# Optimization experiments

Measured on AMD Instinct MI355X. Metric: run time of the kernel, lower is better.

Reference implementation:

```python
import jax, jax.numpy as jnp
import numpy as np

T, H, I = 4096, 4096, 11008  # tokens, hidden_size, intermediate_size
QMAX = 127.0


def setup_inputs() -> dict:
    key = jax.random.key(0)
    k0, k1, k2, k3, k4 = jax.random.split(key, 5)
    x = jax.random.normal(k0, (T, H), dtype=jnp.float32)
    # int8 weights stored as float32 integer values in [-127, 127]
    wq_gate_up = jnp.round(jnp.clip(jax.random.normal(k1, (2 * I, H), dtype=jnp.float32) * 30.0, -QMAX, QMAX))
    s_gate_up = jax.random.uniform(k2, (2 * I,), dtype=jnp.float32, minval=5e-4, maxval=2e-3)
    wq_down = jnp.round(jnp.clip(jax.random.normal(k3, (H, I), dtype=jnp.float32) * 30.0, -QMAX, QMAX))
    s_down = jax.random.uniform(k4, (H,), dtype=jnp.float32, minval=5e-4, maxval=2e-3)
    return {"x": x, "wq_gate_up": wq_gate_up, "s_gate_up": s_gate_up,
            "wq_down": wq_down, "s_down": s_down}


def reference(x, wq_gate_up, s_gate_up, wq_down, s_down):
    # --- quantize activations (per-tensor dynamic int8) ---
    x_scale = jnp.max(jnp.abs(x)) / QMAX
    qx = jnp.clip(jnp.round(x / x_scale), -QMAX, QMAX)  # integer-valued f32 (simulated int8)

    # --- gate_up_proj: int8 GEMM (int32 accumulate simulated in f32) ---
    acc = qx @ wq_gate_up.T                             # [T, 2I]
    gate_up = acc * (x_scale * s_gate_up)               # dequant: per-tensor act * per-channel weight scale

    # --- DequantSiluAndMulQuant: silu(gate) * up, then dynamic requant ---
    gate, up = jnp.split(gate_up, 2, axis=-1)           # [T, I] each
    h = jax.nn.silu(gate) * up
    h_scale = jnp.max(jnp.abs(h)) / QMAX
    qh = jnp.clip(jnp.round(h / h_scale), -QMAX, QMAX)

    # --- down_proj: int8 GEMM + dequant ---
    out = (qh @ wq_down.T) * (h_scale * s_down)         # [T, H]
    return out, h_scale
```

## Files before the change

### kernel.cpp

```cpp
#include <hip/hip_runtime.h>

#define T_DIM 4096
#define K1    4096
#define I_DIM 11008
#define QMAXF 127.0f

typedef int v4i  __attribute__((ext_vector_type(4)));
typedef int v16i __attribute__((ext_vector_type(16)));


__device__ __forceinline__ void gload16(const void* g, void* l) {
  __builtin_amdgcn_global_load_lds((__attribute__((address_space(1))) unsigned int*)(g),
                                   (__attribute__((address_space(3))) unsigned int*)(l),
                                   16, 0, 0);
}

__device__ __forceinline__ int packq(float a, float b, float c, float d) {
  return ((int)a & 255) | (((int)b & 255) << 8) | (((int)c & 255) << 16) | (((int)d & 255) << 24);
}


__global__ void absmax_x_kernel(const float4* __restrict__ x4, unsigned* __restrict__ maxbits, int n4) {
  int tid = blockIdx.x * blockDim.x + threadIdx.x;
  int stride = gridDim.x * blockDim.x;
  float m = 0.f;
  for (int i = tid; i < n4; i += stride) {
    float4 v = x4[i];
    m = fmaxf(m, fmaxf(fmaxf(fabsf(v.x), fabsf(v.y)), fmaxf(fabsf(v.z), fabsf(v.w))));
  }
  #pragma unroll
  for (int off = 32; off; off >>= 1) m = fmaxf(m, __shfl_xor(m, off));
  if ((threadIdx.x & 63) == 0) atomicMax(maxbits, __float_as_uint(m));
}


__global__ void quant_x_kernel(const float4* __restrict__ x4, v4i* __restrict__ q4,
                               const unsigned* __restrict__ scal) {
  const float sx = __uint_as_float(scal[0]) * (1.0f / QMAXF);
  const long i = (long)blockIdx.x * blockDim.x + threadIdx.x;
  v4i o;
  #pragma unroll
  for (int j = 0; j < 4; ++j) {
    float4 v = x4[i * 4 + j];
    float a = fminf(fmaxf(rintf(v.x / sx), -QMAXF), QMAXF);
    float b = fminf(fmaxf(rintf(v.y / sx), -QMAXF), QMAXF);
    float c = fminf(fmaxf(rintf(v.z / sx), -QMAXF), QMAXF);
    float d = fminf(fmaxf(rintf(v.w / sx), -QMAXF), QMAXF);
    o[j] = packq(a, b, c, d);
  }
  q4[i] = o;
}


__global__ void conv_w_kernel(const float4* __restrict__ w4, v4i* __restrict__ q4) {
  const long i = (long)blockIdx.x * blockDim.x + threadIdx.x;
  v4i o;
  #pragma unroll
  for (int j = 0; j < 4; ++j) {
    float4 v = w4[i * 4 + j];
    o[j] = packq(rintf(v.x), rintf(v.y), rintf(v.z), rintf(v.w));
  }
  q4[i] = o;
}


__global__ __launch_bounds__(512, 2)
void gemm1_silu_kernel(const signed char* __restrict__ qx,
                       const signed char* __restrict__ w8,
                       const float* __restrict__ sgu,
                       unsigned* __restrict__ scal,
                       float* __restrict__ hbuf)
{
  __shared__ signed char L[4][32768];

  const int tid  = threadIdx.x;
  const int lane = tid & 63;
  const int wid  = tid >> 6;
  const int wr   = wid >> 1;
  const int wc   = wid & 1;
  const int l31  = lane & 31;
  const int kgl  = lane >> 5;

  const int lin = blockIdx.x;
  const int sw  = (lin & 7) * 172 + (lin >> 3);
  const int brow = (sw & 15) * 256;
  const int bcol = (sw >> 4) * 128;

  const int sr = tid & 255, sk = tid >> 8;
  const signed char* gA = qx + (size_t)(brow + sr) * K1 + sk * 16;
  const int grp = sr >> 6, w = sr & 63;
  const int gcolw = bcol + grp * 32 + (w & 31);
  const size_t srcrow = (w < 32) ? (size_t)gcolw : (size_t)(I_DIM + gcolw);
  const signed char* gB = w8 + srcrow * K1 + sk * 16;
  const int lA = tid * 16;
  const int lB = 16384 + tid * 16;

  const int ab = (wr * 64 + l31) * 16;
  const int bb = 16384 + (wc * 128 + l31) * 16;

  v16i zero = {0};
  v16i acc[2][4];
  #pragma unroll
  for (int m = 0; m < 2; ++m)
    #pragma unroll
    for (int n = 0; n < 4; ++n) acc[m][n] = zero;

  const int nk = K1 / 64;
  #pragma unroll
  for (int t = 0; t < 3; ++t) {
    gload16(gA + t * 64,      &L[t][lA]);
    gload16(gA + t * 64 + 32, &L[t][lA + 8192]);
    gload16(gB + t * 64,      &L[t][lB]);
    gload16(gB + t * 64 + 32, &L[t][lB + 8192]);
  }

  for (int t = 0; t < nk; ++t) {
    if (t + 2 < nk)      asm volatile("s_waitcnt vmcnt(8)" ::: "memory");
    else if (t + 1 < nk) asm volatile("s_waitcnt vmcnt(4)" ::: "memory");
    else                 asm volatile("s_waitcnt vmcnt(0)" ::: "memory");
    __builtin_amdgcn_s_barrier();
    asm volatile("" ::: "memory");
    const signed char* Lb = L[t & 3];
    signed char* Ls = L[(t + 3) & 3];
    const bool st = (t + 3) < nk;
    const int ko = (t + 3) * 64;

    {
      v4i af0, af1, bf0, bf1, bf2, bf3;
      af0 = *(const v4i*)&Lb[kgl * 4096 + ab];
      af1 = *(const v4i*)&Lb[kgl * 4096 + ab + 512];
      bf0 = *(const v4i*)&Lb[kgl * 4096 + bb];
      bf1 = *(const v4i*)&Lb[kgl * 4096 + bb + 512];
      bf2 = *(const v4i*)&Lb[kgl * 4096 + bb + 1024];
      bf3 = *(const v4i*)&Lb[kgl * 4096 + bb + 1536];
      if (st) {
        gload16(gA + ko,      &Ls[lA]);
        gload16(gA + ko + 32, &Ls[lA + 8192]);
      }
      __builtin_amdgcn_s_barrier();
      asm volatile("s_waitcnt lgkmcnt(0)" ::: "memory");
      __builtin_amdgcn_sched_barrier(0);
      __builtin_amdgcn_s_setprio(1);
      acc[0][0] = __builtin_amdgcn_mfma_i32_32x32x32_i8(af0, bf0, acc[0][0], 0, 0, 0);
      acc[0][1] = __builtin_amdgcn_mfma_i32_32x32x32_i8(af0, bf1, acc[0][1], 0, 0, 0);
      acc[0][2] = __builtin_amdgcn_mfma_i32_32x32x32_i8(af0, bf2, acc[0][2], 0, 0, 0);
      acc[0][3] = __builtin_amdgcn_mfma_i32_32x32x32_i8(af0, bf3, acc[0][3], 0, 0, 0);
      acc[1][0] = __builtin_amdgcn_mfma_i32_32x32x32_i8(af1, bf0, acc[1][0], 0, 0, 0);
      acc[1][1] = __builtin_amdgcn_mfma_i32_32x32x32_i8(af1, bf1, acc[1][1], 0, 0, 0);
      acc[1][2] = __builtin_amdgcn_mfma_i32_32x32x32_i8(af1, bf2, acc[1][2], 0, 0, 0);
      acc[1][3] = __builtin_amdgcn_mfma_i32_32x32x32_i8(af1, bf3, acc[1][3], 0, 0, 0);
      __builtin_amdgcn_s_setprio(0);
    }

    {
      v4i af0, af1, bf0, bf1, bf2, bf3;
      af0 = *(const v4i*)&Lb[(2 + kgl) * 4096 + ab];
      af1 = *(const v4i*)&Lb[(2 + kgl) * 4096 + ab + 512];
      bf0 = *(const v4i*)&Lb[(2 + kgl) * 4096 + bb];
      bf1 = *(const v4i*)&Lb[(2 + kgl) * 4096 + bb + 512];
      bf2 = *(const v4i*)&Lb[(2 + kgl) * 4096 + bb + 1024];
      bf3 = *(const v4i*)&Lb[(2 + kgl) * 4096 + bb + 1536];
      if (st) {
        gload16(gB + ko,      &Ls[lB]);
        gload16(gB + ko + 32, &Ls[lB + 8192]);
      }
      __builtin_amdgcn_s_barrier();
      asm volatile("s_waitcnt lgkmcnt(0)" ::: "memory");
      __builtin_amdgcn_sched_barrier(0);
      __builtin_amdgcn_s_setprio(1);
      acc[0][0] = __builtin_amdgcn_mfma_i32_32x32x32_i8(af0, bf0, acc[0][0], 0, 0, 0);
      acc[0][1] = __builtin_amdgcn_mfma_i32_32x32x32_i8(af0, bf1, acc[0][1], 0, 0, 0);
      acc[0][2] = __builtin_amdgcn_mfma_i32_32x32x32_i8(af0, bf2, acc[0][2], 0, 0, 0);
      acc[0][3] = __builtin_amdgcn_mfma_i32_32x32x32_i8(af0, bf3, acc[0][3], 0, 0, 0);
      acc[1][0] = __builtin_amdgcn_mfma_i32_32x32x32_i8(af1, bf0, acc[1][0], 0, 0, 0);
      acc[1][1] = __builtin_amdgcn_mfma_i32_32x32x32_i8(af1, bf1, acc[1][1], 0, 0, 0);
      acc[1][2] = __builtin_amdgcn_mfma_i32_32x32x32_i8(af1, bf2, acc[1][2], 0, 0, 0);
      acc[1][3] = __builtin_amdgcn_mfma_i32_32x32x32_i8(af1, bf3, acc[1][3], 0, 0, 0);
      __builtin_amdgcn_s_setprio(0);
    }
  }

  const float xsc = __uint_as_float(scal[0]) * (1.0f / QMAXF);
  float hmax = 0.f;
  #pragma unroll
  for (int m = 0; m < 2; ++m) {
    const int rbase = brow + wr * 64 + m * 32 + 4 * kgl;
    #pragma unroll
    for (int p = 0; p < 2; ++p) {
      const int col = bcol + (wc * 2 + p) * 32 + l31;
      const float sg = sgu[col] * xsc;
      const float su = sgu[I_DIM + col] * xsc;
      #pragma unroll
      for (int q = 0; q < 16; ++q) {
        const int row = rbase + (q & 3) + 8 * (q >> 2);
        float g = (float)acc[m][2 * p][q] * sg;
        float u = (float)acc[m][2 * p + 1][q] * su;
        float hv = (g / (1.f + expf(-g))) * u;
        hmax = fmaxf(hmax, fabsf(hv));
        hbuf[(size_t)row * I_DIM + col] = hv;
      }
    }
  }
  #pragma unroll
  for (int off = 32; off; off >>= 1) hmax = fmaxf(hmax, __shfl_xor(hmax, off));
  if (lane == 0) atomicMax(scal + 1, __float_as_uint(hmax));
}


__global__ void quant_h_kernel(const float4* __restrict__ h4, v4i* __restrict__ q4,
                               const unsigned* __restrict__ scal) {
  const float hs = __uint_as_float(scal[1]) * (1.0f / QMAXF);
  const long i = (long)blockIdx.x * blockDim.x + threadIdx.x;
  v4i o;
  #pragma unroll
  for (int j = 0; j < 4; ++j) {
    float4 v = h4[i * 4 + j];
    float a = fminf(fmaxf(rintf(v.x / hs), -QMAXF), QMAXF);
    float b = fminf(fmaxf(rintf(v.y / hs), -QMAXF), QMAXF);
    float c = fminf(fmaxf(rintf(v.z / hs), -QMAXF), QMAXF);
    float d = fminf(fmaxf(rintf(v.w / hs), -QMAXF), QMAXF);
    o[j] = packq(a, b, c, d);
  }
  q4[i] = o;
}

__global__ void hscale_out_kernel(const unsigned* __restrict__ scal, float* __restrict__ dst) {
  dst[0] = __uint_as_float(scal[1]) * (1.0f / QMAXF);
}


__global__ __launch_bounds__(512, 2)
void gemm2_kernel(const signed char* __restrict__ qh,
                  const signed char* __restrict__ w8,
                  const float* __restrict__ sdn,
                  const unsigned* __restrict__ scal,
                  float* __restrict__ out)
{
  __shared__ signed char L[4][32768];

  const int tid  = threadIdx.x;
  const int lane = tid & 63;
  const int wid  = tid >> 6;
  const int wr   = wid >> 1;
  const int wc   = wid & 1;
  const int l31  = lane & 31;
  const int kgl  = lane >> 5;

  const int lin = blockIdx.x;
  const int sw  = (lin & 7) * 32 + (lin >> 3);
  const int brow = (sw & 15) * 256;
  const int bcol = (sw >> 4) * 256;

  const int sr = tid & 255, sk = tid >> 8;
  const signed char* gA = qh + (size_t)(brow + sr) * I_DIM + sk * 16;
  const signed char* gB = w8 + (size_t)(bcol + sr) * I_DIM + sk * 16;
  const int lA = tid * 16;
  const int lB = 16384 + tid * 16;

  const int ab = (wr * 64 + l31) * 16;
  const int bb = 16384 + (wc * 128 + l31) * 16;

  v16i zero = {0};
  v16i acc[2][4];
  #pragma unroll
  for (int m = 0; m < 2; ++m)
    #pragma unroll
    for (int n = 0; n < 4; ++n) acc[m][n] = zero;

  const int nk = I_DIM / 64;
  #pragma unroll
  for (int t = 0; t < 3; ++t) {
    gload16(gA + t * 64,      &L[t][lA]);
    gload16(gA + t * 64 + 32, &L[t][lA + 8192]);
    gload16(gB + t * 64,      &L[t][lB]);
    gload16(gB + t * 64 + 32, &L[t][lB + 8192]);
  }

  for (int t = 0; t < nk; ++t) {
    if (t + 2 < nk)      asm volatile("s_waitcnt vmcnt(8)" ::: "memory");
    else if (t + 1 < nk) asm volatile("s_waitcnt vmcnt(4)" ::: "memory");
    else                 asm volatile("s_waitcnt vmcnt(0)" ::: "memory");
    __builtin_amdgcn_s_barrier();
    asm volatile("" ::: "memory");
    const signed char* Lb = L[t & 3];
    signed char* Ls = L[(t + 3) & 3];
    const bool st = (t + 3) < nk;
    const int ko = (t + 3) * 64;

    {
      v4i af0, af1, bf0, bf1, bf2, bf3;
      af0 = *(const v4i*)&Lb[kgl * 4096 + ab];
      af1 = *(const v4i*)&Lb[kgl * 4096 + ab + 512];
      bf0 = *(const v4i*)&Lb[kgl * 4096 + bb];
      bf1 = *(const v4i*)&Lb[kgl * 4096 + bb + 512];
      bf2 = *(const v4i*)&Lb[kgl * 4096 + bb + 1024];
      bf3 = *(const v4i*)&Lb[kgl * 4096 + bb + 1536];
      if (st) {
        gload16(gA + ko,      &Ls[lA]);
        gload16(gA + ko + 32, &Ls[lA + 8192]);
      }
      __builtin_amdgcn_s_barrier();
      asm volatile("s_waitcnt lgkmcnt(0)" ::: "memory");
      __builtin_amdgcn_sched_barrier(0);
      __builtin_amdgcn_s_setprio(1);
      acc[0][0] = __builtin_amdgcn_mfma_i32_32x32x32_i8(af0, bf0, acc[0][0], 0, 0, 0);
      acc[0][1] = __builtin_amdgcn_mfma_i32_32x32x32_i8(af0, bf1, acc[0][1], 0, 0, 0);
      acc[0][2] = __builtin_amdgcn_mfma_i32_32x32x32_i8(af0, bf2, acc[0][2], 0, 0, 0);
      acc[0][3] = __builtin_amdgcn_mfma_i32_32x32x32_i8(af0, bf3, acc[0][3], 0, 0, 0);
      acc[1][0] = __builtin_amdgcn_mfma_i32_32x32x32_i8(af1, bf0, acc[1][0], 0, 0, 0);
      acc[1][1] = __builtin_amdgcn_mfma_i32_32x32x32_i8(af1, bf1, acc[1][1], 0, 0, 0);
      acc[1][2] = __builtin_amdgcn_mfma_i32_32x32x32_i8(af1, bf2, acc[1][2], 0, 0, 0);
      acc[1][3] = __builtin_amdgcn_mfma_i32_32x32x32_i8(af1, bf3, acc[1][3], 0, 0, 0);
      __builtin_amdgcn_s_setprio(0);
    }

    {
      v4i af0, af1, bf0, bf1, bf2, bf3;
      af0 = *(const v4i*)&Lb[(2 + kgl) * 4096 + ab];
      af1 = *(const v4i*)&Lb[(2 + kgl) * 4096 + ab + 512];
      bf0 = *(const v4i*)&Lb[(2 + kgl) * 4096 + bb];
      bf1 = *(const v4i*)&Lb[(2 + kgl) * 4096 + bb + 512];
      bf2 = *(const v4i*)&Lb[(2 + kgl) * 4096 + bb + 1024];
      bf3 = *(const v4i*)&Lb[(2 + kgl) * 4096 + bb + 1536];
      if (st) {
        gload16(gB + ko,      &Ls[lB]);
        gload16(gB + ko + 32, &Ls[lB + 8192]);
      }
      __builtin_amdgcn_s_barrier();
      asm volatile("s_waitcnt lgkmcnt(0)" ::: "memory");
      __builtin_amdgcn_sched_barrier(0);
      __builtin_amdgcn_s_setprio(1);
      acc[0][0] = __builtin_amdgcn_mfma_i32_32x32x32_i8(af0, bf0, acc[0][0], 0, 0, 0);
      acc[0][1] = __builtin_amdgcn_mfma_i32_32x32x32_i8(af0, bf1, acc[0][1], 0, 0, 0);
      acc[0][2] = __builtin_amdgcn_mfma_i32_32x32x32_i8(af0, bf2, acc[0][2], 0, 0, 0);
      acc[0][3] = __builtin_amdgcn_mfma_i32_32x32x32_i8(af0, bf3, acc[0][3], 0, 0, 0);
      acc[1][0] = __builtin_amdgcn_mfma_i32_32x32x32_i8(af1, bf0, acc[1][0], 0, 0, 0);
      acc[1][1] = __builtin_amdgcn_mfma_i32_32x32x32_i8(af1, bf1, acc[1][1], 0, 0, 0);
      acc[1][2] = __builtin_amdgcn_mfma_i32_32x32x32_i8(af1, bf2, acc[1][2], 0, 0, 0);
      acc[1][3] = __builtin_amdgcn_mfma_i32_32x32x32_i8(af1, bf3, acc[1][3], 0, 0, 0);
      __builtin_amdgcn_s_setprio(0);
    }
  }

  const float hsc = __uint_as_float(scal[1]) * (1.0f / QMAXF);
  #pragma unroll
  for (int m = 0; m < 2; ++m) {
    const int rbase = brow + wr * 64 + m * 32 + 4 * kgl;
    #pragma unroll
    for (int n = 0; n < 4; ++n) {
      const int col = bcol + wc * 128 + n * 32 + l31;
      const float s = sdn[col] * hsc;
      #pragma unroll
      for (int q = 0; q < 16; ++q) {
        const int row = rbase + (q & 3) + 8 * (q >> 2);
        out[(size_t)row * K1 + col] = (float)acc[m][n][q] * s;
      }
    }
  }
}


extern "C" void kernel_launch(void* const* d_in, const int* in_sizes, int n_in,
                              void* d_out, int out_size, void* d_ws, size_t ws_size,
                              hipStream_t stream) {
  (void)in_sizes; (void)n_in; (void)out_size; (void)ws_size;
  const float* x   = (const float*)d_in[0];
  const float* wgu = (const float*)d_in[1];
  const float* sgu = (const float*)d_in[2];
  const float* wdn = (const float*)d_in[3];
  const float* sdn = (const float*)d_in[4];
  float* out = (float*)d_out;
  char* ws = (char*)d_ws;

  signed char* qx  = (signed char*)(ws + 0LL);
  signed char* w8g = (signed char*)(ws + 16777216LL);
  signed char* w8d = (signed char*)(ws + 106954752LL);
  signed char* qh  = (signed char*)(ws + 152043520LL);
  float*       hb  = (float*)      (ws + 197132288LL);
  unsigned*    scal= (unsigned*)   (ws + 377487360LL);

  hipMemsetAsync(scal, 0, 256, stream);
  absmax_x_kernel<<<2048, 256, 0, stream>>>((const float4*)x, scal, T_DIM * K1 / 4);
  quant_x_kernel<<<4096, 256, 0, stream>>>((const float4*)x, (v4i*)qx, scal);
  conv_w_kernel<<<22016, 256, 0, stream>>>((const float4*)wgu, (v4i*)w8g);
  conv_w_kernel<<<11008, 256, 0, stream>>>((const float4*)wdn, (v4i*)w8d);

  gemm1_silu_kernel<<<1376, 512, 0, stream>>>(qx, w8g, sgu, scal, hb);

  quant_h_kernel<<<11008, 256, 0, stream>>>((const float4*)hb, (v4i*)qh, scal);
  hscale_out_kernel<<<1, 1, 0, stream>>>(scal, out + (size_t)T_DIM * K1);

  gemm2_kernel<<<256, 512, 0, stream>>>(qh, w8d, sdn, scal, out);
}
```

Baseline: 1.163 ms.

## Unroll K loop by four with static LDS buffers and one barrier per tile

```diff
diff --git a/kernel.cpp b/kernel.cpp
--- a/kernel.cpp
+++ b/kernel.cpp
@@ -18,6 +18,8 @@
 __device__ __forceinline__ int packq(float a, float b, float c, float d) {
   return ((int)a & 255) | (((int)b & 255) << 8) | (((int)c & 255) << 16) | (((int)d & 255) << 24);
 }
+
+#define MFMA32(A, B, C) __builtin_amdgcn_mfma_i32_32x32x32_i8(A, B, C, 0, 0, 0)
 
 
 __global__ void absmax_x_kernel(const float4* __restrict__ x4, unsigned* __restrict__ maxbits, int n4) {
@@ -63,6 +65,51 @@
   q4[i] = o;
 }
 
+
+#define TILE_BODY(U, W, S, ACCSTMTS)                                        \
+  {                                                                         \
+    asm volatile("s_waitcnt vmcnt(" #W ")" ::: "memory");                   \
+    __builtin_amdgcn_s_barrier();                                           \
+    asm volatile("" ::: "memory");                                          \
+    if (S) {                                                                \
+      gload16(gAs + (U) * 64,      &L[((U) + 3) & 3][lA]);                  \
+      gload16(gAs + (U) * 64 + 32, &L[((U) + 3) & 3][lA + 8192]);           \
+      gload16(gBs + (U) * 64,      &L[((U) + 3) & 3][lB]);                  \
+      gload16(gBs + (U) * 64 + 32, &L[((U) + 3) & 3][lB + 8192]);           \
+    }                                                                       \
+    const signed char* Lb = L[(U)];                                         \
+    v4i a0 = *(const v4i*)&Lb[kgl * 4096 + ab];                             \
+    v4i a1 = *(const v4i*)&Lb[kgl * 4096 + ab + 512];                       \
+    v4i b0 = *(const v4i*)&Lb[kgl * 4096 + bb];                             \
+    v4i b1 = *(const v4i*)&Lb[kgl * 4096 + bb + 512];                       \
+    v4i b2 = *(const v4i*)&Lb[kgl * 4096 + bb + 1024];                      \
+    v4i b3 = *(const v4i*)&Lb[kgl * 4096 + bb + 1536];                      \
+    v4i a2 = *(const v4i*)&Lb[(2 + kgl) * 4096 + ab];                       \
+    v4i a3 = *(const v4i*)&Lb[(2 + kgl) * 4096 + ab + 512];                 \
+    v4i b4 = *(const v4i*)&Lb[(2 + kgl) * 4096 + bb];                       \
+    v4i b5 = *(const v4i*)&Lb[(2 + kgl) * 4096 + bb + 512];                 \
+    v4i b6 = *(const v4i*)&Lb[(2 + kgl) * 4096 + bb + 1024];                \
+    v4i b7 = *(const v4i*)&Lb[(2 + kgl) * 4096 + bb + 1536];                \
+    ACCSTMTS                                                                \
+  }
+
+#define ACC_16(acc)                                                         \
+    acc[0][0] = MFMA32(a0, b0, acc[0][0]);                                  \
+    acc[0][1] = MFMA32(a0, b1, acc[0][1]);                                  \
+    acc[0][2] = MFMA32(a0, b2, acc[0][2]);                                  \
+    acc[0][3] = MFMA32(a0, b3, acc[0][3]);                                  \
+    acc[1][0] = MFMA32(a1, b0, acc[1][0]);                                  \
+    acc[1][1] = MFMA32(a1, b1, acc[1][1]);                                  \
+    acc[1][2] = MFMA32(a1, b2, acc[1][2]);                                  \
+    acc[1][3] = MFMA32(a1, b3, acc[1][3]);                                  \
+    acc[0][0] = MFMA32(a2, b4, acc[0][0]);                                  \
+    acc[0][1] = MFMA32(a2, b5, acc[0][1]);                                  \
+    acc[0][2] = MFMA32(a2, b6, acc[0][2]);                                  \
+    acc[0][3] = MFMA32(a2, b7, acc[0][3]);                                  \
+    acc[1][0] = MFMA32(a3, b4, acc[1][0]);                                  \
+    acc[1][1] = MFMA32(a3, b5, acc[1][1]);                                  \
+    acc[1][2] = MFMA32(a3, b6, acc[1][2]);                                  \
+    acc[1][3] = MFMA32(a3, b7, acc[1][3]);
 
 __global__ __launch_bounds__(512, 2)
 void gemm1_silu_kernel(const signed char* __restrict__ qx,
@@ -114,71 +161,20 @@
     gload16(gB + t * 64 + 32, &L[t][lB + 8192]);
   }
 
-  for (int t = 0; t < nk; ++t) {
-    if (t + 2 < nk)      asm volatile("s_waitcnt vmcnt(8)" ::: "memory");
-    else if (t + 1 < nk) asm volatile("s_waitcnt vmcnt(4)" ::: "memory");
-    else                 asm volatile("s_waitcnt vmcnt(0)" ::: "memory");
-    __builtin_amdgcn_s_barrier();
-    asm volatile("" ::: "memory");
-    const signed char* Lb = L[t & 3];
-    signed char* Ls = L[(t + 3) & 3];
-    const bool st = (t + 3) < nk;
-    const int ko = (t + 3) * 64;
-
-    {
-      v4i af0, af1, bf0, bf1, bf2, bf3;
-      af0 = *(const v4i*)&Lb[kgl * 4096 + ab];
-      af1 = *(const v4i*)&Lb[kgl * 4096 + ab + 512];
-      bf0 = *(const v4i*)&Lb[kgl * 4096 + bb];
-      bf1 = *(const v4i*)&Lb[kgl * 4096 + bb + 512];
-      bf2 = *(const v4i*)&Lb[kgl * 4096 + bb + 1024];
-      bf3 = *(const v4i*)&Lb[kgl * 4096 + bb + 1536];
-      if (st) {
-        gload16(gA + ko,      &Ls[lA]);
-        gload16(gA + ko + 32, &Ls[lA + 8192]);
-      }
-      __builtin_amdgcn_s_barrier();
-      asm volatile("s_waitcnt lgkmcnt(0)" ::: "memory");
-      __builtin_amdgcn_sched_barrier(0);
-      __builtin_amdgcn_s_setprio(1);
-      acc[0][0] = __builtin_amdgcn_mfma_i32_32x32x32_i8(af0, bf0, acc[0][0], 0, 0, 0);
-      acc[0][1] = __builtin_amdgcn_mfma_i32_32x32x32_i8(af0, bf1, acc[0][1], 0, 0, 0);
-      acc[0][2] = __builtin_amdgcn_mfma_i32_32x32x32_i8(af0, bf2, acc[0][2], 0, 0, 0);
-      acc[0][3] = __builtin_amdgcn_mfma_i32_32x32x32_i8(af0, bf3, acc[0][3], 0, 0, 0);
-      acc[1][0] = __builtin_amdgcn_mfma_i32_32x32x32_i8(af1, bf0, acc[1][0], 0, 0, 0);
-      acc[1][1] = __builtin_amdgcn_mfma_i32_32x32x32_i8(af1, bf1, acc[1][1], 0, 0, 0);
-      acc[1][2] = __builtin_amdgcn_mfma_i32_32x32x32_i8(af1, bf2, acc[1][2], 0, 0, 0);
-      acc[1][3] = __builtin_amdgcn_mfma_i32_32x32x32_i8(af1, bf3, acc[1][3], 0, 0, 0);
-      __builtin_amdgcn_s_setprio(0);
-    }
-
-    {
-      v4i af0, af1, bf0, bf1, bf2, bf3;
-      af0 = *(const v4i*)&Lb[(2 + kgl) * 4096 + ab];
-      af1 = *(const v4i*)&Lb[(2 + kgl) * 4096 + ab + 512];
-      bf0 = *(const v4i*)&Lb[(2 + kgl) * 4096 + bb];
-      bf1 = *(const v4i*)&Lb[(2 + kgl) * 4096 + bb + 512];
-      bf2 = *(const v4i*)&Lb[(2 + kgl) * 4096 + bb + 1024];
-      bf3 = *(const v4i*)&Lb[(2 + kgl) * 4096 + bb + 1536];
-      if (st) {
-        gload16(gB + ko,      &Ls[lB]);
-        gload16(gB + ko + 32, &Ls[lB + 8192]);
-      }
-      __builtin_amdgcn_s_barrier();
-      asm volatile("s_waitcnt lgkmcnt(0)" ::: "memory");
-      __builtin_amdgcn_sched_barrier(0);
-      __builtin_amdgcn_s_setprio(1);
-      acc[0][0] = __builtin_amdgcn_mfma_i32_32x32x32_i8(af0, bf0, acc[0][0], 0, 0, 0);
-      acc[0][1] = __builtin_amdgcn_mfma_i32_32x32x32_i8(af0, bf1, acc[0][1], 0, 0, 0);
-      acc[0][2] = __builtin_amdgcn_mfma_i32_32x32x32_i8(af0, bf2, acc[0][2], 0, 0, 0);
-      acc[0][3] = __builtin_amdgcn_mfma_i32_32x32x32_i8(af0, bf3, acc[0][3], 0, 0, 0);
-      acc[1][0] = __builtin_amdgcn_mfma_i32_32x32x32_i8(af1, bf0, acc[1][0], 0, 0, 0);
-      acc[1][1] = __builtin_amdgcn_mfma_i32_32x32x32_i8(af1, bf1, acc[1][1], 0, 0, 0);
-      acc[1][2] = __builtin_amdgcn_mfma_i32_32x32x32_i8(af1, bf2, acc[1][2], 0, 0, 0);
-      acc[1][3] = __builtin_amdgcn_mfma_i32_32x32x32_i8(af1, bf3, acc[1][3], 0, 0, 0);
-      __builtin_amdgcn_s_setprio(0);
-    }
-  }
+  const signed char* gAs = gA + 192;
+  const signed char* gBs = gB + 192;
+
+  for (int it = 0; it < nk / 4 - 1; ++it) {
+    TILE_BODY(0, 8, true, ACC_16(acc))
+    TILE_BODY(1, 8, true, ACC_16(acc))
+    TILE_BODY(2, 8, true, ACC_16(acc))
+    TILE_BODY(3, 8, true, ACC_16(acc))
+    gAs += 256; gBs += 256;
+  }
+  TILE_BODY(0, 8, true,  ACC_16(acc))
+  TILE_BODY(1, 8, false, ACC_16(acc))
+  TILE_BODY(2, 4, false, ACC_16(acc))
+  TILE_BODY(3, 0, false, ACC_16(acc))
 
   const float xsc = __uint_as_float(scal[0]) * (1.0f / QMAXF);
   float hmax = 0.f;
@@ -276,71 +272,20 @@
     gload16(gB + t * 64 + 32, &L[t][lB + 8192]);
   }
 
-  for (int t = 0; t < nk; ++t) {
-    if (t + 2 < nk)      asm volatile("s_waitcnt vmcnt(8)" ::: "memory");
-    else if (t + 1 < nk) asm volatile("s_waitcnt vmcnt(4)" ::: "memory");
-    else                 asm volatile("s_waitcnt vmcnt(0)" ::: "memory");
-    __builtin_amdgcn_s_barrier();
-    asm volatile("" ::: "memory");
-    const signed char* Lb = L[t & 3];
-    signed char* Ls = L[(t + 3) & 3];
-    const bool st = (t + 3) < nk;
-    const int ko = (t + 3) * 64;
-
-    {
-      v4i af0, af1, bf0, bf1, bf2, bf3;
-      af0 = *(const v4i*)&Lb[kgl * 4096 + ab];
-      af1 = *(const v4i*)&Lb[kgl * 4096 + ab + 512];
-      bf0 = *(const v4i*)&Lb[kgl * 4096 + bb];
-      bf1 = *(const v4i*)&Lb[kgl * 4096 + bb + 512];
-      bf2 = *(const v4i*)&Lb[kgl * 4096 + bb + 1024];
-      bf3 = *(const v4i*)&Lb[kgl * 4096 + bb + 1536];
-      if (st) {
-        gload16(gA + ko,      &Ls[lA]);
-        gload16(gA + ko + 32, &Ls[lA + 8192]);
-      }
-      __builtin_amdgcn_s_barrier();
-      asm volatile("s_waitcnt lgkmcnt(0)" ::: "memory");
-      __builtin_amdgcn_sched_barrier(0);
-      __builtin_amdgcn_s_setprio(1);
-      acc[0][0] = __builtin_amdgcn_mfma_i32_32x32x32_i8(af0, bf0, acc[0][0], 0, 0, 0);
-      acc[0][1] = __builtin_amdgcn_mfma_i32_32x32x32_i8(af0, bf1, acc[0][1], 0, 0, 0);
-      acc[0][2] = __builtin_amdgcn_mfma_i32_32x32x32_i8(af0, bf2, acc[0][2], 0, 0, 0);
-      acc[0][3] = __builtin_amdgcn_mfma_i32_32x32x32_i8(af0, bf3, acc[0][3], 0, 0, 0);
-      acc[1][0] = __builtin_amdgcn_mfma_i32_32x32x32_i8(af1, bf0, acc[1][0], 0, 0, 0);
-      acc[1][1] = __builtin_amdgcn_mfma_i32_32x32x32_i8(af1, bf1, acc[1][1], 0, 0, 0);
-      acc[1][2] = __builtin_amdgcn_mfma_i32_32x32x32_i8(af1, bf2, acc[1][2], 0, 0, 0);
-      acc[1][3] = __builtin_amdgcn_mfma_i32_32x32x32_i8(af1, bf3, acc[1][3], 0, 0, 0);
-      __builtin_amdgcn_s_setprio(0);
-    }
-
-    {
-      v4i af0, af1, bf0, bf1, bf2, bf3;
-      af0 = *(const v4i*)&Lb[(2 + kgl) * 4096 + ab];
-      af1 = *(const v4i*)&Lb[(2 + kgl) * 4096 + ab + 512];
-      bf0 = *(const v4i*)&Lb[(2 + kgl) * 4096 + bb];
-      bf1 = *(const v4i*)&Lb[(2 + kgl) * 4096 + bb + 512];
-      bf2 = *(const v4i*)&Lb[(2 + kgl) * 4096 + bb + 1024];
-      bf3 = *(const v4i*)&Lb[(2 + kgl) * 4096 + bb + 1536];
-      if (st) {
-        gload16(gB + ko,      &Ls[lB]);
-        gload16(gB + ko + 32, &Ls[lB + 8192]);
-      }
-      __builtin_amdgcn_s_barrier();
-      asm volatile("s_waitcnt lgkmcnt(0)" ::: "memory");
-      __builtin_amdgcn_sched_barrier(0);
-      __builtin_amdgcn_s_setprio(1);
-      acc[0][0] = __builtin_amdgcn_mfma_i32_32x32x32_i8(af0, bf0, acc[0][0], 0, 0, 0);
-      acc[0][1] = __builtin_amdgcn_mfma_i32_32x32x32_i8(af0, bf1, acc[0][1], 0, 0, 0);
-      acc[0][2] = __builtin_amdgcn_mfma_i32_32x32x32_i8(af0, bf2, acc[0][2], 0, 0, 0);
-      acc[0][3] = __builtin_amdgcn_mfma_i32_32x32x32_i8(af0, bf3, acc[0][3], 0, 0, 0);
-      acc[1][0] = __builtin_amdgcn_mfma_i32_32x32x32_i8(af1, bf0, acc[1][0], 0, 0, 0);
-      acc[1][1] = __builtin_amdgcn_mfma_i32_32x32x32_i8(af1, bf1, acc[1][1], 0, 0, 0);
-      acc[1][2] = __builtin_amdgcn_mfma_i32_32x32x32_i8(af1, bf2, acc[1][2], 0, 0, 0);
-      acc[1][3] = __builtin_amdgcn_mfma_i32_32x32x32_i8(af1, bf3, acc[1][3], 0, 0, 0);
-      __builtin_amdgcn_s_setprio(0);
-    }
-  }
+  const signed char* gAs = gA + 192;
+  const signed char* gBs = gB + 192;
+
+  for (int it = 0; it < nk / 4 - 1; ++it) {
+    TILE_BODY(0, 8, true, ACC_16(acc))
+    TILE_BODY(1, 8, true, ACC_16(acc))
+    TILE_BODY(2, 8, true, ACC_16(acc))
+    TILE_BODY(3, 8, true, ACC_16(acc))
+    gAs += 256; gBs += 256;
+  }
+  TILE_BODY(0, 8, true,  ACC_16(acc))
+  TILE_BODY(1, 8, false, ACC_16(acc))
+  TILE_BODY(2, 4, false, ACC_16(acc))
+  TILE_BODY(3, 0, false, ACC_16(acc))
 
   const float hsc = __uint_as_float(scal[1]) * (1.0f / QMAXF);
   #pragma unroll
```

After: 1.280 ms. +10.0%, slower.
